# Kernel optimization log

Measured on AMD Instinct MI355X. Metric: run time of the kernel, lower is better.

## Reference

```python
import jax, jax.numpy as jnp
import numpy as np

N_NODES = 50000
N_EDGES = 800000
D = 128


def gcn_conv(x, W, b, src, dst, num_nodes):
    """PyG GCNConv: x @ W, add self-loops, symmetric normalization, scatter-add, + bias."""
    x = x @ W  # [N, out]
    loop = jnp.arange(num_nodes, dtype=src.dtype)
    s = jnp.concatenate([src, loop])  # [E+N]
    d = jnp.concatenate([dst, loop])
    w = jnp.ones(s.shape[0], x.dtype)  # edge_weight=None -> ones (self-loop fill=1)
    deg = jax.ops.segment_sum(w, d, num_segments=num_nodes)  # [N]
    dinv = jnp.where(deg > 0, jax.lax.rsqrt(deg), 0.0)
    norm = dinv[s] * dinv[d]  # [E+N]
    out = jax.ops.segment_sum(x[s] * norm[:, None], d, num_segments=num_nodes)
    return out + b


def setup_inputs() -> dict:
    key = jax.random.key(0)
    ks = jax.random.split(key, 8)
    sc = 1.0 / np.sqrt(D)
    x = jax.random.normal(ks[0], (N_NODES, D), dtype=jnp.float32)
    edge_index = jax.random.randint(ks[1], (2, N_EDGES), 0, N_NODES)
    W1 = jax.random.normal(ks[2], (D, D), dtype=jnp.float32) * sc
    W2 = jax.random.normal(ks[3], (D, D), dtype=jnp.float32) * sc
    W3 = jax.random.normal(ks[4], (D, D), dtype=jnp.float32) * sc
    b1 = jnp.zeros((D,), jnp.float32)
    b2 = jnp.zeros((D,), jnp.float32)
    b3 = jnp.zeros((D,), jnp.float32)
    return {"x": x, "edge_index": edge_index, "W1": W1, "b1": b1,
            "W2": W2, "b2": b2, "W3": W3, "b3": b3}


def reference(x, edge_index, W1, b1, W2, b2, W3, b3):
    src, dst = edge_index[0], edge_index[1]
    n = x.shape[0]
    x = jax.nn.relu(gcn_conv(x, W1, b1, src, dst, n))
    x = jax.nn.relu(gcn_conv(x, W2, b2, src, dst, n))
    return gcn_conv(x, W3, b3, src, dst, n)
```

## Files before the change

kernel.cpp:

```cpp
#include <hip/hip_runtime.h>
#include <hip/hip_fp16.h>
#include <math.h>

#define D 128

typedef __attribute__((ext_vector_type(8))) _Float16 half8;
typedef __attribute__((ext_vector_type(4))) float f32x4;


__global__ void count_rank_kernel(const int* __restrict__ dst, int* __restrict__ cnt,
                                  int* __restrict__ rank, int E) {
    int e0 = (blockIdx.x * blockDim.x + threadIdx.x) * 8;
    if (e0 + 7 < E) {
        int4 da = *(const int4*)(dst + e0);
        int4 db = *(const int4*)(dst + e0 + 4);
        int4 ra, rb;
        ra.x = atomicAdd(&cnt[da.x], 1);
        ra.y = atomicAdd(&cnt[da.y], 1);
        ra.z = atomicAdd(&cnt[da.z], 1);
        ra.w = atomicAdd(&cnt[da.w], 1);
        rb.x = atomicAdd(&cnt[db.x], 1);
        rb.y = atomicAdd(&cnt[db.y], 1);
        rb.z = atomicAdd(&cnt[db.z], 1);
        rb.w = atomicAdd(&cnt[db.w], 1);
        *(int4*)(rank + e0)     = ra;
        *(int4*)(rank + e0 + 4) = rb;
    } else {
        for (int e = e0; e < E; ++e) rank[e] = atomicAdd(&cnt[dst[e]], 1);
    }
}

__global__ __launch_bounds__(1024) void scan_kernel(const int* __restrict__ cnt,
                                                    int* __restrict__ rowptr,
                                                    float* __restrict__ dinv,
                                                    int N) {
    __shared__ int wsum[16];
    __shared__ int carry_s;
    int tid  = threadIdx.x;
    int lane = tid & 63;
    int wid  = tid >> 6;
    if (tid == 0) carry_s = 0;
    __syncthreads();
    for (int base = 0; base < N; base += 4096) {
        int i = base + tid * 4;
        int4 v = make_int4(0, 0, 0, 0);
        if (i + 3 < N) v = *(const int4*)(cnt + i);
        else {
            if (i + 0 < N) v.x = cnt[i + 0];
            if (i + 1 < N) v.y = cnt[i + 1];
            if (i + 2 < N) v.z = cnt[i + 2];
            if (i + 3 < N) v.w = cnt[i + 3];
        }
        int s0 = v.x, s1 = s0 + v.y, s2 = s1 + v.z, s3 = s2 + v.w;
        int sc = s3;
        #pragma unroll
        for (int off = 1; off < 64; off <<= 1) {
            int t = __shfl_up(sc, off, 64);
            if (lane >= off) sc += t;
        }
        if (lane == 63) wsum[wid] = sc;
        __syncthreads();
        if (tid < 16) {
            int w = wsum[tid];
            #pragma unroll
            for (int off = 1; off < 16; off <<= 1) {
                int t = __shfl_up(w, off, 64);
                if (tid >= off) w += t;
            }
            wsum[tid] = w;
        }
        __syncthreads();
        int waveoff = (wid > 0) ? wsum[wid - 1] : 0;
        int excl = carry_s + waveoff + (sc - s3);
        if (i + 0 < N) { rowptr[i + 0] = excl;      dinv[i + 0] = rsqrtf((float)v.x + 1.0f); }
        if (i + 1 < N) { rowptr[i + 1] = excl + s0; dinv[i + 1] = rsqrtf((float)v.y + 1.0f); }
        if (i + 2 < N) { rowptr[i + 2] = excl + s1; dinv[i + 2] = rsqrtf((float)v.z + 1.0f); }
        if (i + 3 < N) { rowptr[i + 3] = excl + s2; dinv[i + 3] = rsqrtf((float)v.w + 1.0f); }
        __syncthreads();
        if (tid == 0) carry_s += wsum[15];
        __syncthreads();
    }
    if (tid == 0) rowptr[N] = carry_s;
}

__global__ void fill_kernel(const int* __restrict__ src, const int* __restrict__ dst,
                            const int* __restrict__ rank, const int* __restrict__ rowptr,
                            int* __restrict__ col, int E) {
    int e0 = (blockIdx.x * blockDim.x + threadIdx.x) * 8;
    if (e0 + 7 < E) {
        int4 da = *(const int4*)(dst + e0);
        int4 db = *(const int4*)(dst + e0 + 4);
        int4 ra = *(const int4*)(rank + e0);
        int4 rb = *(const int4*)(rank + e0 + 4);
        int4 sa = *(const int4*)(src + e0);
        int4 sb = *(const int4*)(src + e0 + 4);
        col[rowptr[da.x] + ra.x] = sa.x;
        col[rowptr[da.y] + ra.y] = sa.y;
        col[rowptr[da.z] + ra.z] = sa.z;
        col[rowptr[da.w] + ra.w] = sa.w;
        col[rowptr[db.x] + rb.x] = sb.x;
        col[rowptr[db.y] + rb.y] = sb.y;
        col[rowptr[db.z] + rb.z] = sb.z;
        col[rowptr[db.w] + rb.w] = sb.w;
    } else {
        for (int e = e0; e < E; ++e) col[rowptr[dst[e]] + rank[e]] = src[e];
    }
}


__global__ void convw_kernel(const float* __restrict__ W1, const float* __restrict__ W2,
                             const float* __restrict__ W3, __half* __restrict__ WhT) {
    int i = blockIdx.x * blockDim.x + threadIdx.x;
    int l = i >> 14;
    int j = i & 16383;
    int n = j >> 7, k = j & 127;
    const float* W = (l == 0) ? W1 : (l == 1) ? W2 : W3;
    WhT[(size_t)i] = __float2half(W[(size_t)k * D + n]);
}


__global__ __launch_bounds__(256) void gemm_mfma_f32(const float* __restrict__ X,
                                                     const __half* __restrict__ WhT,
                                                     const float* __restrict__ dinv,
                                                     __half* __restrict__ Y, int M) {
    int tid  = threadIdx.x;
    int wave = tid >> 6;
    int lane = tid & 63;
    int quad = lane >> 4;
    int l16  = lane & 15;
    int m0   = blockIdx.x * 64 + wave * 16;
    if (m0 >= M) return;

    f32x4 acc[8];
    #pragma unroll
    for (int t = 0; t < 8; ++t) acc[t] = (f32x4)0.0f;

    const float* xrow = X + (size_t)(m0 + l16) * D;

    #pragma unroll
    for (int ks = 0; ks < 4; ++ks) {
        int k0 = ks * 32 + quad * 8;
        float4 x0 = *(const float4*)(xrow + k0);
        float4 x1 = *(const float4*)(xrow + k0 + 4);
        half8 a;
        a[0] = (_Float16)x0.x; a[1] = (_Float16)x0.y;
        a[2] = (_Float16)x0.z; a[3] = (_Float16)x0.w;
        a[4] = (_Float16)x1.x; a[5] = (_Float16)x1.y;
        a[6] = (_Float16)x1.z; a[7] = (_Float16)x1.w;
        #pragma unroll
        for (int t = 0; t < 8; ++t) {
            half8 b = *(const half8*)(WhT + (size_t)(t * 16 + l16) * D + k0);
            acc[t] = __builtin_amdgcn_mfma_f32_16x16x32_f16(a, b, acc[t], 0, 0, 0);
        }
    }

    float4 dv = *(const float4*)(dinv + m0 + quad * 4);
    float dvs[4] = {dv.x, dv.y, dv.z, dv.w};
    #pragma unroll
    for (int t = 0; t < 8; ++t) {
        #pragma unroll
        for (int r = 0; r < 4; ++r) {
            int grow = m0 + quad * 4 + r;
            Y[(size_t)grow * D + t * 16 + l16] = __float2half(acc[t][r] * dvs[r]);
        }
    }
}


__global__ __launch_bounds__(256) void fused_agg_gemm(const __half* __restrict__ ysin,
                                                      const int* __restrict__ rowptr,
                                                      const int* __restrict__ col,
                                                      const float* __restrict__ dinv,
                                                      const float* __restrict__ bias,
                                                      const __half* __restrict__ WhT,
                                                      __half* __restrict__ ysout, int M) {
    int tid  = threadIdx.x;
    int wave = tid >> 6;
    int lane = tid & 63;
    int quad = lane >> 4;
    int l16  = lane & 15;
    int m0   = blockIdx.x * 64 + wave * 16;
    if (m0 >= M) return;

    int n = m0 + l16;
    int s = rowptr[n], e = rowptr[n + 1];

    float acc[4][8];
    #pragma unroll
    for (int ks = 0; ks < 4; ++ks)
        #pragma unroll
        for (int j = 0; j < 8; ++j) acc[ks][j] = 0.0f;

    const __half* basep = ysin + quad * 8;
    for (int i = s; i < e; ++i) {
        int c = col[i];
        const __half* r = basep + (size_t)c * D;
        half8 v0 = *(const half8*)(r);
        half8 v1 = *(const half8*)(r + 32);
        half8 v2 = *(const half8*)(r + 64);
        half8 v3 = *(const half8*)(r + 96);
        #pragma unroll
        for (int j = 0; j < 8; ++j) {
            acc[0][j] += (float)v0[j];
            acc[1][j] += (float)v1[j];
            acc[2][j] += (float)v2[j];
            acc[3][j] += (float)v3[j];
        }
    }
    {
        const __half* r = basep + (size_t)n * D;
        half8 v0 = *(const half8*)(r);
        half8 v1 = *(const half8*)(r + 32);
        half8 v2 = *(const half8*)(r + 64);
        half8 v3 = *(const half8*)(r + 96);
        #pragma unroll
        for (int j = 0; j < 8; ++j) {
            acc[0][j] += (float)v0[j];
            acc[1][j] += (float)v1[j];
            acc[2][j] += (float)v2[j];
            acc[3][j] += (float)v3[j];
        }
    }

    float dv = dinv[n];
    half8 a[4];
    #pragma unroll
    for (int ks = 0; ks < 4; ++ks) {
        const float* bp = bias + ks * 32 + quad * 8;
        float4 bq0 = *(const float4*)(bp);
        float4 bq1 = *(const float4*)(bp + 4);
        float t0 = fmaxf(bq0.x + dv * acc[ks][0], 0.f);
        float t1 = fmaxf(bq0.y + dv * acc[ks][1], 0.f);
        float t2 = fmaxf(bq0.z + dv * acc[ks][2], 0.f);
        float t3 = fmaxf(bq0.w + dv * acc[ks][3], 0.f);
        float t4 = fmaxf(bq1.x + dv * acc[ks][4], 0.f);
        float t5 = fmaxf(bq1.y + dv * acc[ks][5], 0.f);
        float t6 = fmaxf(bq1.z + dv * acc[ks][6], 0.f);
        float t7 = fmaxf(bq1.w + dv * acc[ks][7], 0.f);
        a[ks][0] = (_Float16)t0; a[ks][1] = (_Float16)t1;
        a[ks][2] = (_Float16)t2; a[ks][3] = (_Float16)t3;
        a[ks][4] = (_Float16)t4; a[ks][5] = (_Float16)t5;
        a[ks][6] = (_Float16)t6; a[ks][7] = (_Float16)t7;
    }

    f32x4 o[8];
    #pragma unroll
    for (int t = 0; t < 8; ++t) o[t] = (f32x4)0.0f;
    #pragma unroll
    for (int ks = 0; ks < 4; ++ks) {
        int k0 = ks * 32 + quad * 8;
        #pragma unroll
        for (int t = 0; t < 8; ++t) {
            half8 b = *(const half8*)(WhT + (size_t)(t * 16 + l16) * D + k0);
            o[t] = __builtin_amdgcn_mfma_f32_16x16x32_f16(a[ks], b, o[t], 0, 0, 0);
        }
    }

    float4 dvo = *(const float4*)(dinv + m0 + quad * 4);
    float dvs[4] = {dvo.x, dvo.y, dvo.z, dvo.w};
    #pragma unroll
    for (int t = 0; t < 8; ++t) {
        #pragma unroll
        for (int r = 0; r < 4; ++r) {
            int grow = m0 + quad * 4 + r;
            ysout[(size_t)grow * D + t * 16 + l16] = __float2half(o[t][r] * dvs[r]);
        }
    }
}


__device__ __forceinline__ void acc_h8(float2 a[4], half8 v) {
    a[0].x += (float)v[0]; a[0].y += (float)v[1];
    a[1].x += (float)v[2]; a[1].y += (float)v[3];
    a[2].x += (float)v[4]; a[2].y += (float)v[5];
    a[3].x += (float)v[6]; a[3].y += (float)v[7];
}

__global__ __launch_bounds__(256) void aggregate_final(const __half* __restrict__ ys,
                                                       const int* __restrict__ rowptr,
                                                       const int* __restrict__ col,
                                                       const float* __restrict__ dinv,
                                                       const float* __restrict__ b,
                                                       float* __restrict__ outf,
                                                       int N) {
    int gwave = (blockIdx.x * blockDim.x + threadIdx.x) >> 6;
    int lane  = threadIdx.x & 63;
    int g     = lane >> 4;
    int l16   = lane & 15;
    if (gwave >= N) return;
    int row = gwave;
    int s = rowptr[row], e = rowptr[row + 1];

    float2 a[4];
    a[0] = a[1] = a[2] = a[3] = make_float2(0.f, 0.f);

    for (int base = s; base < e; base += 64) {
        int idx = base + lane;
        int myc = (idx < e) ? col[idx] : 0;
        int nb  = min(64, e - base);
        int nb4 = nb & ~3;
        #pragma unroll 4
        for (int j = 0; j < nb4; j += 4) {
            int c = __shfl(myc, j + g);
            half8 v = *(const half8*)(ys + (size_t)c * D + (l16 << 3));
            acc_h8(a, v);
        }
        int rem = nb - nb4;
        if (rem) {
            int jj = nb4 + min(g, rem - 1);
            int c = __shfl(myc, jj);
            half8 v = *(const half8*)(ys + (size_t)c * D + (l16 << 3));
            float m = (g < rem) ? 1.f : 0.f;
            a[0].x += m * (float)v[0]; a[0].y += m * (float)v[1];
            a[1].x += m * (float)v[2]; a[1].y += m * (float)v[3];
            a[2].x += m * (float)v[4]; a[2].y += m * (float)v[5];
            a[3].x += m * (float)v[6]; a[3].y += m * (float)v[7];
        }
    }

    #pragma unroll
    for (int k = 0; k < 4; ++k) {
        a[k].x += __shfl_xor(a[k].x, 16, 64);
        a[k].y += __shfl_xor(a[k].y, 16, 64);
        a[k].x += __shfl_xor(a[k].x, 32, 64);
        a[k].y += __shfl_xor(a[k].y, 32, 64);
    }

    half8 us = *(const half8*)(ys + (size_t)row * D + (l16 << 3));
    acc_h8(a, us);

    float dv = dinv[row];
    float4 b0 = *(const float4*)(b + (l16 << 3));
    float4 b1 = *(const float4*)(b + (l16 << 3) + 4);
    float r0 = b0.x + dv * a[0].x, r1 = b0.y + dv * a[0].y;
    float r2 = b0.z + dv * a[1].x, r3 = b0.w + dv * a[1].y;
    float r4 = b1.x + dv * a[2].x, r5 = b1.y + dv * a[2].y;
    float r6 = b1.z + dv * a[3].x, r7 = b1.w + dv * a[3].y;

    if (g == 0)
        *(float4*)(outf + (size_t)row * D + (l16 << 3)) = make_float4(r0, r1, r2, r3);
    else if (g == 1)
        *(float4*)(outf + (size_t)row * D + (l16 << 3) + 4) = make_float4(r4, r5, r6, r7);
}


extern "C" void kernel_launch(void* const* d_in, const int* in_sizes, int n_in,
                              void* d_out, int out_size, void* d_ws, size_t ws_size,
                              hipStream_t stream) {
    const float* x   = (const float*)d_in[0];
    const int*   ei  = (const int*)d_in[1];
    const float* W1  = (const float*)d_in[2];
    const float* b1  = (const float*)d_in[3];
    const float* W2  = (const float*)d_in[4];
    const float* b2  = (const float*)d_in[5];
    const float* W3  = (const float*)d_in[6];
    const float* b3  = (const float*)d_in[7];
    float* out = (float*)d_out;

    const int N = in_sizes[0] / D;
    const int E = in_sizes[1] / 2;
    const int* src = ei;
    const int* dst = ei + E;

    char* ws = (char*)d_ws;
    size_t off = 0;
    auto alloc = [&](size_t bytes) {
        void* p = ws + off;
        off = (off + bytes + 255) & ~(size_t)255;
        return p;
    };
    __half* ysA   = (__half*)alloc((size_t)N * D * sizeof(__half));
    __half* ysB   = (__half*)alloc((size_t)N * D * sizeof(__half));
    int*   cnt    = (int*)alloc((size_t)N * sizeof(int));
    int*   rowptr = (int*)alloc((size_t)(N + 1) * sizeof(int));
    float* dinv   = (float*)alloc((size_t)N * sizeof(float));
    int*   rank   = (int*)alloc((size_t)E * sizeof(int));
    int*   col    = (int*)alloc((size_t)E * sizeof(int));
    __half* WhT   = (__half*)alloc((size_t)3 * D * D * sizeof(__half));
    (void)ws_size; (void)n_in; (void)out_size;

    convw_kernel<<<(3 * D * D + 255) / 256, 256, 0, stream>>>(W1, W2, W3, WhT);

    hipMemsetAsync(cnt, 0, (size_t)N * sizeof(int), stream);
    const int egrid = ((E + 7) / 8 + 255) / 256;
    count_rank_kernel<<<egrid, 256, 0, stream>>>(dst, cnt, rank, E);
    scan_kernel<<<1, 1024, 0, stream>>>(cnt, rowptr, dinv, N);
    fill_kernel<<<egrid, 256, 0, stream>>>(src, dst, rank, rowptr, col, E);

    const int tile_grid = (N + 63) / 64;
    const int agg_grid  = (N * 64 + 255) / 256;

    gemm_mfma_f32<<<tile_grid, 256, 0, stream>>>(x, WhT, dinv, ysA, N);
    fused_agg_gemm<<<tile_grid, 256, 0, stream>>>(ysA, rowptr, col, dinv, b1, WhT + 16384, ysB, N);
    fused_agg_gemm<<<tile_grid, 256, 0, stream>>>(ysB, rowptr, col, dinv, b2, WhT + 32768, ysA, N);
    aggregate_final<<<agg_grid, 256, 0, stream>>>(ysA, rowptr, col, dinv, b3, out, N);
}
```

Baseline: 338.0 us.

## Split fused aggregation-GEMM across four waves by K slice with LDS reduction

Each block now handles 16 rows instead of 64, and each of the four waves gathers only a 32-column K slice of the neighbor features and runs its partial MFMA. Waves 1 to 3 write their partial products to shared memory, and wave 0 sums them and stores the output. The neighbor loop is unrolled by 4, with out-of-range slots redirected to a zeroed padding row at index N, which lets more loads be in flight. This cuts per-thread register use and gives four times as many blocks to hide gather latency. In exchange it adds shared memory traffic, a block barrier and a serial reduction in wave 0.

```diff
diff --git a/kernel.cpp b/kernel.cpp
--- a/kernel.cpp
+++ b/kernel.cpp
@@ -174,96 +174,83 @@
                                                       const float* __restrict__ bias,
                                                       const __half* __restrict__ WhT,
                                                       __half* __restrict__ ysout, int M) {
+    __shared__ float red[3][16][129];
     int tid  = threadIdx.x;
-    int wave = tid >> 6;
+    int w    = tid >> 6;
     int lane = tid & 63;
     int quad = lane >> 4;
     int l16  = lane & 15;
-    int m0   = blockIdx.x * 64 + wave * 16;
+    int m0   = blockIdx.x * 16;
     if (m0 >= M) return;
 
     int n = m0 + l16;
     int s = rowptr[n], e = rowptr[n + 1];
-
-    float acc[4][8];
-    #pragma unroll
-    for (int ks = 0; ks < 4; ++ks)
-        #pragma unroll
-        for (int j = 0; j < 8; ++j) acc[ks][j] = 0.0f;
-
-    const __half* basep = ysin + quad * 8;
-    for (int i = s; i < e; ++i) {
-        int c = col[i];
-        const __half* r = basep + (size_t)c * D;
-        half8 v0 = *(const half8*)(r);
-        half8 v1 = *(const half8*)(r + 32);
-        half8 v2 = *(const half8*)(r + 64);
-        half8 v3 = *(const half8*)(r + 96);
-        #pragma unroll
-        for (int j = 0; j < 8; ++j) {
-            acc[0][j] += (float)v0[j];
-            acc[1][j] += (float)v1[j];
-            acc[2][j] += (float)v2[j];
-            acc[3][j] += (float)v3[j];
+    int k0 = w * 32 + quad * 8;
+    const __half* basep = ysin + k0;
+
+    float acc[8];
+    #pragma unroll
+    for (int j = 0; j < 8; ++j) acc[j] = 0.0f;
+
+    for (int i = s; i < e; i += 4) {
+        #pragma unroll
+        for (int u = 0; u < 4; ++u) {
+            int idx = i + u;
+            int c = (idx < e) ? col[idx] : M;
+            half8 v = *(const half8*)(basep + (size_t)c * D);
+            #pragma unroll
+            for (int j = 0; j < 8; ++j) acc[j] += (float)v[j];
         }
     }
     {
-        const __half* r = basep + (size_t)n * D;
-        half8 v0 = *(const half8*)(r);
-        half8 v1 = *(const half8*)(r + 32);
-        half8 v2 = *(const half8*)(r + 64);
-        half8 v3 = *(const half8*)(r + 96);
-        #pragma unroll
-        for (int j = 0; j < 8; ++j) {
-            acc[0][j] += (float)v0[j];
-            acc[1][j] += (float)v1[j];
-            acc[2][j] += (float)v2[j];
-            acc[3][j] += (float)v3[j];
-        }
+        half8 v = *(const half8*)(basep + (size_t)n * D);
+        #pragma unroll
+        for (int j = 0; j < 8; ++j) acc[j] += (float)v[j];
     }
 
     float dv = dinv[n];
-    half8 a[4];
-    #pragma unroll
-    for (int ks = 0; ks < 4; ++ks) {
-        const float* bp = bias + ks * 32 + quad * 8;
-        float4 bq0 = *(const float4*)(bp);
-        float4 bq1 = *(const float4*)(bp + 4);
-        float t0 = fmaxf(bq0.x + dv * acc[ks][0], 0.f);
-        float t1 = fmaxf(bq0.y + dv * acc[ks][1], 0.f);
-        float t2 = fmaxf(bq0.z + dv * acc[ks][2], 0.f);
-        float t3 = fmaxf(bq0.w + dv * acc[ks][3], 0.f);
-        float t4 = fmaxf(bq1.x + dv * acc[ks][4], 0.f);
-        float t5 = fmaxf(bq1.y + dv * acc[ks][5], 0.f);
-        float t6 = fmaxf(bq1.z + dv * acc[ks][6], 0.f);
-        float t7 = fmaxf(bq1.w + dv * acc[ks][7], 0.f);
-        a[ks][0] = (_Float16)t0; a[ks][1] = (_Float16)t1;
-        a[ks][2] = (_Float16)t2; a[ks][3] = (_Float16)t3;
-        a[ks][4] = (_Float16)t4; a[ks][5] = (_Float16)t5;
-        a[ks][6] = (_Float16)t6; a[ks][7] = (_Float16)t7;
-    }
+    const float* bp = bias + k0;
+    float4 bq0 = *(const float4*)(bp);
+    float4 bq1 = *(const float4*)(bp + 4);
+    half8 a;
+    a[0] = (_Float16)fmaxf(bq0.x + dv * acc[0], 0.f);
+    a[1] = (_Float16)fmaxf(bq0.y + dv * acc[1], 0.f);
+    a[2] = (_Float16)fmaxf(bq0.z + dv * acc[2], 0.f);
+    a[3] = (_Float16)fmaxf(bq0.w + dv * acc[3], 0.f);
+    a[4] = (_Float16)fmaxf(bq1.x + dv * acc[4], 0.f);
+    a[5] = (_Float16)fmaxf(bq1.y + dv * acc[5], 0.f);
+    a[6] = (_Float16)fmaxf(bq1.z + dv * acc[6], 0.f);
+    a[7] = (_Float16)fmaxf(bq1.w + dv * acc[7], 0.f);
 
     f32x4 o[8];
     #pragma unroll
     for (int t = 0; t < 8; ++t) o[t] = (f32x4)0.0f;
     #pragma unroll
-    for (int ks = 0; ks < 4; ++ks) {
-        int k0 = ks * 32 + quad * 8;
+    for (int t = 0; t < 8; ++t) {
+        half8 b = *(const half8*)(WhT + (size_t)(t * 16 + l16) * D + k0);
+        o[t] = __builtin_amdgcn_mfma_f32_16x16x32_f16(a, b, o[t], 0, 0, 0);
+    }
+
+    if (w > 0) {
+        #pragma unroll
+        for (int t = 0; t < 8; ++t)
+            #pragma unroll
+            for (int r = 0; r < 4; ++r)
+                red[w - 1][quad * 4 + r][t * 16 + l16] = o[t][r];
+    }
+    __syncthreads();
+    if (w == 0) {
+        float4 dvo = *(const float4*)(dinv + m0 + quad * 4);
+        float dvs[4] = {dvo.x, dvo.y, dvo.z, dvo.w};
         #pragma unroll
         for (int t = 0; t < 8; ++t) {
-            half8 b = *(const half8*)(WhT + (size_t)(t * 16 + l16) * D + k0);
-            o[t] = __builtin_amdgcn_mfma_f32_16x16x32_f16(a[ks], b, o[t], 0, 0, 0);
-        }
-    }
-
-    float4 dvo = *(const float4*)(dinv + m0 + quad * 4);
-    float dvs[4] = {dvo.x, dvo.y, dvo.z, dvo.w};
-    #pragma unroll
-    for (int t = 0; t < 8; ++t) {
-        #pragma unroll
-        for (int r = 0; r < 4; ++r) {
-            int grow = m0 + quad * 4 + r;
-            ysout[(size_t)grow * D + t * 16 + l16] = __float2half(o[t][r] * dvs[r]);
+            #pragma unroll
+            for (int r = 0; r < 4; ++r) {
+                int m = quad * 4 + r;
+                float sum = o[t][r] + red[0][m][t * 16 + l16]
+                          + red[1][m][t * 16 + l16] + red[2][m][t * 16 + l16];
+                ysout[(size_t)(m0 + m) * D + t * 16 + l16] = __float2half(sum * dvs[r]);
+            }
         }
     }
 }
@@ -369,8 +356,8 @@
         off = (off + bytes + 255) & ~(size_t)255;
         return p;
     };
-    __half* ysA   = (__half*)alloc((size_t)N * D * sizeof(__half));
-    __half* ysB   = (__half*)alloc((size_t)N * D * sizeof(__half));
+    __half* ysA   = (__half*)alloc((size_t)(N + 1) * D * sizeof(__half));
+    __half* ysB   = (__half*)alloc((size_t)(N + 1) * D * sizeof(__half));
     int*   cnt    = (int*)alloc((size_t)N * sizeof(int));
     int*   rowptr = (int*)alloc((size_t)(N + 1) * sizeof(int));
     float* dinv   = (float*)alloc((size_t)N * sizeof(float));
@@ -382,16 +369,19 @@
     convw_kernel<<<(3 * D * D + 255) / 256, 256, 0, stream>>>(W1, W2, W3, WhT);
 
     hipMemsetAsync(cnt, 0, (size_t)N * sizeof(int), stream);
+    hipMemsetAsync(ysA + (size_t)N * D, 0, (size_t)D * sizeof(__half), stream);
+    hipMemsetAsync(ysB + (size_t)N * D, 0, (size_t)D * sizeof(__half), stream);
     const int egrid = ((E + 7) / 8 + 255) / 256;
     count_rank_kernel<<<egrid, 256, 0, stream>>>(dst, cnt, rank, E);
     scan_kernel<<<1, 1024, 0, stream>>>(cnt, rowptr, dinv, N);
     fill_kernel<<<egrid, 256, 0, stream>>>(src, dst, rank, rowptr, col, E);
 
-    const int tile_grid = (N + 63) / 64;
-    const int agg_grid  = (N * 64 + 255) / 256;
-
-    gemm_mfma_f32<<<tile_grid, 256, 0, stream>>>(x, WhT, dinv, ysA, N);
-    fused_agg_gemm<<<tile_grid, 256, 0, stream>>>(ysA, rowptr, col, dinv, b1, WhT + 16384, ysB, N);
-    fused_agg_gemm<<<tile_grid, 256, 0, stream>>>(ysB, rowptr, col, dinv, b2, WhT + 32768, ysA, N);
+    const int gemm_grid  = (N + 63) / 64;
+    const int fused_grid = (N + 15) / 16;
+    const int agg_grid   = (N * 64 + 255) / 256;
+
+    gemm_mfma_f32<<<gemm_grid, 256, 0, stream>>>(x, WhT, dinv, ysA, N);
+    fused_agg_gemm<<<fused_grid, 256, 0, stream>>>(ysA, rowptr, col, dinv, b1, WhT + 16384, ysB, N);
+    fused_agg_gemm<<<fused_grid, 256, 0, stream>>>(ysB, rowptr, col, dinv, b2, WhT + 32768, ysA, N);
     aggregate_final<<<agg_grid, 256, 0, stream>>>(ysA, rowptr, col, dinv, b3, out, N);
 }
```

Result: slower. 357.1 us (+5.6%).
